# Kernel tuning notes

Hardware: AMD Instinct MI355X
Metric: run time of the kernel (lower is better)

The kernel has to match this reference:

```python
import jax, jax.numpy as jnp
import numpy as np

B, S, H, E, K = 2, 2048, 1024, 8, 2
CAP_FACTOR = 1.5

def setup_inputs() -> dict:
    key = jax.random.key(0)
    ks = jax.random.split(key, 8)
    sd1 = 1.0 / np.sqrt(H)
    sd2 = 1.0 / np.sqrt(H + E)
    return {
        'hidden_states': jax.random.normal(ks[0], (B, S, H), dtype=jnp.float32),
        'w1': jax.random.normal(ks[1], (H, H), dtype=jnp.float32) * sd1,
        'b1': jnp.zeros((H,), jnp.float32),
        'w2': jax.random.normal(ks[2], (H, E), dtype=jnp.float32) * sd1,
        'b2': jnp.zeros((E,), jnp.float32),
        'wc1': jax.random.normal(ks[3], (H + E, H), dtype=jnp.float32) * sd2,
        'bc1': jnp.zeros((H,), jnp.float32),
        'wc2': jax.random.normal(ks[4], (H, E), dtype=jnp.float32) * sd1,
        'bc2': jnp.zeros((E,), jnp.float32),
        'cache_hit_rates': jax.random.uniform(ks[5], (E,), dtype=jnp.float32),
    }

def reference(hidden_states, w1, b1, w2, b2, wc1, bc1, wc2, bc2, cache_hit_rates):
    b, s, h = hidden_states.shape
    # router MLP: Linear -> ReLU -> Linear
    router_logits = jax.nn.relu(hidden_states @ w1 + b1) @ w2 + b2  # [B,S,E]
    # cache-aware adjustment
    avg_features = hidden_states.mean(axis=1)  # [B,H]
    combined = jnp.concatenate(
        [avg_features, jnp.broadcast_to(cache_hit_rates[None, :], (b, E))], axis=-1)
    adj = jnp.tanh(jax.nn.relu(combined @ wc1 + bc1) @ wc2 + bc2)  # [B,E]
    router_logits = router_logits + adj[:, None, :]
    router_probs = jax.nn.softmax(router_logits, axis=-1)  # [B,S,E]
    top_k_probs, top_k_indices = jax.lax.top_k(router_probs, K)  # [B,S,K]
    top_k_probs = top_k_probs / (top_k_probs.sum(axis=-1, keepdims=True) + 1e-8)
    capacity = int(b * s * CAP_FACTOR * K / E)
    # flatten in (b, s, k) order to replicate serial capacity counters
    N = b * s * K
    e_flat = top_k_indices.reshape(N)
    p_flat = top_k_probs.reshape(N)
    tok = jnp.arange(N) // K  # token index b*S+s
    onehot = jax.nn.one_hot(e_flat, E, dtype=jnp.int32)  # [N,E] small
    prior = jnp.cumsum(onehot, axis=0) - onehot  # exclusive count per expert
    pos = prior[jnp.arange(N), e_flat]  # slot within expert
    keep = pos < capacity
    posc = jnp.minimum(pos, capacity - 1)
    val = keep.astype(router_probs.dtype)
    dispatch = jnp.zeros((b * s, E, capacity), router_probs.dtype)
    dispatch = dispatch.at[tok, e_flat, posc].add(val).reshape(b, s, E, capacity)
    combine = jnp.zeros((b * s, E, capacity), router_probs.dtype)
    combine = combine.at[tok, e_flat, posc].add(val * p_flat).reshape(b, s, E, capacity)
    # load balancing aux loss
    router_prob_per_expert = router_probs.mean(axis=(0, 1))  # [E]
    expert_usage_rate = onehot.astype(router_probs.dtype).mean(axis=0)  # [E]
    aux_loss = jnp.sum(router_prob_per_expert * expert_usage_rate) * E
    return dispatch, combine, router_probs, aux_loss
```

## Files before the change

### kernel.cpp

```cpp
#include <hip/hip_runtime.h>
#include <hip/hip_bf16.h>

#define BB 2
#define SS 2048
#define HH 1024
#define EE 8
#define KK 2
#define CAP 1536
#define NTOK (BB * SS)
#define NASSIGN (NTOK * KK)

#define WS_PSUM   0
#define WS_AVG    8
#define WS_HC     2056
#define WS_ADJ    4104
#define WS_P1     4120
#define WS_P2     8216
#define WS_IDX    12312
#define WS_LOGITS 16408
#define WS_ZERO_BYTES 16448
#define WS_BF16_BYTE 196704
#define WS_H_BYTE (WS_BF16_BYTE + 31457280)
#define WS_NEED (WS_H_BYTE + 16777216ull)

using short8 = __attribute__((ext_vector_type(8))) short;
using u16x8  = __attribute__((ext_vector_type(8))) unsigned short;
using f32x4  = __attribute__((ext_vector_type(4))) float;

__device__ __forceinline__ unsigned short f2bf(float f) {
  unsigned u = __float_as_uint(f);
  unsigned r = (u + 0x7fffu + ((u >> 16) & 1u)) >> 16;
  return (unsigned short)r;
}
__device__ __forceinline__ float bf2f(unsigned short h) {
  return __uint_as_float((unsigned)h << 16);
}
__device__ __forceinline__ void split3(float x, unsigned short& h,
                                       unsigned short& m, unsigned short& l) {
  h = f2bf(x);
  float r = x - bf2f(h);
  m = f2bf(r);
  l = f2bf(r - bf2f(m));
}

__device__ __forceinline__ void gload_lds16(const void* g, void* l) {
  __builtin_amdgcn_global_load_lds(
      (const __attribute__((address_space(1))) void*)g,
      (__attribute__((address_space(3))) void*)l, 16, 0, 0);
}

__global__ void k_prep_x(const float* __restrict__ x, unsigned short* __restrict__ Xh,
                         unsigned short* __restrict__ Xm, unsigned short* __restrict__ Xl) {
  int i = (blockIdx.x * 256 + threadIdx.x) * 4;
  float4 v = *(const float4*)&x[i];
  unsigned short h[4], m[4], l[4];
  split3(v.x, h[0], m[0], l[0]);
  split3(v.y, h[1], m[1], l[1]);
  split3(v.z, h[2], m[2], l[2]);
  split3(v.w, h[3], m[3], l[3]);
  *(ushort4*)&Xh[i] = make_ushort4(h[0], h[1], h[2], h[3]);
  *(ushort4*)&Xm[i] = make_ushort4(m[0], m[1], m[2], m[3]);
  *(ushort4*)&Xl[i] = make_ushort4(l[0], l[1], l[2], l[3]);
}

__global__ __launch_bounds__(256) void k_prep_w(const float* __restrict__ w1,
    unsigned short* __restrict__ Wh, unsigned short* __restrict__ Wm,
    unsigned short* __restrict__ Wl) {
  __shared__ unsigned short Th[64 * 65], Tm[64 * 65], Tl[64 * 65];
  int tid = threadIdx.x;
  int k0 = blockIdx.x * 64, n0 = blockIdx.y * 64;
  for (int i = 0; i < 16; ++i) {
    int e = i * 256 + tid;
    int k = e >> 6, n = e & 63;
    float v = w1[(size_t)(k0 + k) * HH + n0 + n];
    unsigned short h, m, l;
    split3(v, h, m, l);
    Th[n * 65 + k] = h; Tm[n * 65 + k] = m; Tl[n * 65 + k] = l;
  }
  __syncthreads();
  for (int i = 0; i < 16; ++i) {
    int e = i * 256 + tid;
    int n = e >> 6, k = e & 63;
    size_t o = (size_t)(n0 + n) * HH + k0 + k;
    Wh[o] = Th[n * 65 + k]; Wm[o] = Tm[n * 65 + k]; Wl[o] = Tl[n * 65 + k];
  }
}

__global__ void k_avg(const float* __restrict__ x, float* __restrict__ avg) {
  int h = blockIdx.x * 256 + threadIdx.x;
  int s0 = blockIdx.y * 128;
  int b = blockIdx.z;
  const float* p = x + (size_t)b * SS * HH + (size_t)s0 * HH + h;
  float s = 0.f;
  for (int i = 0; i < 128; ++i) s += p[(size_t)i * HH];
  atomicAdd(&avg[b * HH + h], s);
}

__global__ void k_hc(const float* __restrict__ avg, const float* __restrict__ chr,
                     const float* __restrict__ wc1, float* __restrict__ hc_raw) {
  int j = blockIdx.x * 256 + threadIdx.x;
  int c = blockIdx.y;
  int b = blockIdx.z;
  const float invS = 1.0f / SS;
  float acc = 0.f;
  const float* a = avg + b * HH;
  for (int i = c * 128; i < c * 128 + 128; ++i)
    acc += (a[i] * invS) * wc1[(size_t)i * HH + j];
  if (c == 7)
    for (int i = 0; i < EE; ++i)
      acc += chr[i] * wc1[(size_t)(HH + i) * HH + j];
  atomicAdd(&hc_raw[b * HH + j], acc);
}

__global__ void k_adj(const float* __restrict__ hc_raw, const float* __restrict__ bc1,
                      const float* __restrict__ wc2, const float* __restrict__ bc2,
                      float* __restrict__ adj) {
  int b = blockIdx.x;
  int tid = threadIdx.x;
  float part[EE] = {};
  for (int j = tid; j < HH; j += 256) {
    float v = fmaxf(hc_raw[b * HH + j] + bc1[j], 0.f);
    for (int e = 0; e < EE; ++e) part[e] += v * wc2[j * EE + e];
  }
  for (int m = 1; m < 64; m <<= 1)
    for (int e = 0; e < EE; ++e) part[e] += __shfl_xor(part[e], m);
  __shared__ float red[4][EE];
  int wave = tid >> 6, lane = tid & 63;
  if (lane == 0)
    for (int e = 0; e < EE; ++e) red[wave][e] = part[e];
  __syncthreads();
  if (tid < EE) {
    float s = bc2[tid];
    for (int w = 0; w < 4; ++w) s += red[w][tid];
    adj[b * EE + tid] = tanhf(s);
  }
}

#define BM 128
#define BN 64
#define BK 32
#define ZF4_PER_BLOCK 49152
__global__ __launch_bounds__(256) void k_gemm_mfma(
    const unsigned short* __restrict__ Xh, const unsigned short* __restrict__ Xm,
    const unsigned short* __restrict__ Xl,
    const unsigned short* __restrict__ Wh, const unsigned short* __restrict__ Wm,
    const unsigned short* __restrict__ Wl,
    const float* __restrict__ b1, float* __restrict__ hbuf,
    f32x4* __restrict__ zout) {
  __shared__ unsigned short As[3][BM * BK];
  __shared__ unsigned short Bs[3][BN * BK];
  __shared__ float b1s[BN];
  int tid = threadIdx.x;
  int m0 = blockIdx.x * BM, n0 = blockIdx.y * BN;
  if (tid < BN) b1s[tid] = b1[n0 + tid];

  int bid = blockIdx.y * gridDim.x + blockIdx.x;
  f32x4* zp = zout + (size_t)bid * ZF4_PER_BLOCK;
  const f32x4 z4 = {0.f, 0.f, 0.f, 0.f};

  int lane = tid & 63, wave = tid >> 6;
  int wm = wave & 1, wn = wave >> 1;
  int q = lane >> 4, mr = lane & 15;
  int lr = lane >> 2, lq = lane & 3;

  f32x4 acc[4][2] = {};

  const unsigned short* Ag[3] = {Xh, Xm, Xl};
  const unsigned short* Bg[3] = {Wh, Wm, Wl};

  for (int k0 = 0; k0 < HH; k0 += BK) {
    __syncthreads();
#pragma unroll
    for (int j = 0; j < 6; ++j) {
      int i = wave + 4 * j;
      int s = i >> 3, g = i & 7;
      const unsigned short* gp =
          Ag[s] + (size_t)(m0 + g * 16 + lr) * HH + k0 + lq * 8;
      gload_lds16(gp, &As[s][g * 512]);
    }
#pragma unroll
    for (int j = 0; j < 3; ++j) {
      int i = wave + 4 * j;
      int s = i >> 2, g = i & 3;
      const unsigned short* gp =
          Bg[s] + (size_t)(n0 + g * 16 + lr) * HH + k0 + lq * 8;
      gload_lds16(gp, &Bs[s][g * 512]);
    }
    __syncthreads();

    {
      int ki = k0 >> 5;
      f32x4* zb = zp + ki * (256 * 6) + tid;
#pragma unroll
      for (int j = 0; j < 6; ++j) __builtin_nontemporal_store(z4, &zb[j * 256]);
    }

    short8 af[3][4], bf[3][2];
#pragma unroll
    for (int s = 0; s < 3; ++s) {
#pragma unroll
      for (int mi = 0; mi < 4; ++mi)
        af[s][mi] = *(const short8*)&As[s][(wm * 64 + mi * 16 + mr) * BK + q * 8];
#pragma unroll
      for (int ni = 0; ni < 2; ++ni)
        bf[s][ni] = *(const short8*)&Bs[s][(wn * 32 + ni * 16 + mr) * BK + q * 8];
    }
#pragma unroll
    for (int mi = 0; mi < 4; ++mi)
#pragma unroll
      for (int ni = 0; ni < 2; ++ni) {
        f32x4 c = acc[mi][ni];
        c = __builtin_amdgcn_mfma_f32_16x16x32_bf16(af[0][mi], bf[0][ni], c, 0, 0, 0);
        c = __builtin_amdgcn_mfma_f32_16x16x32_bf16(af[0][mi], bf[1][ni], c, 0, 0, 0);
        c = __builtin_amdgcn_mfma_f32_16x16x32_bf16(af[1][mi], bf[0][ni], c, 0, 0, 0);
        c = __builtin_amdgcn_mfma_f32_16x16x32_bf16(af[0][mi], bf[2][ni], c, 0, 0, 0);
        c = __builtin_amdgcn_mfma_f32_16x16x32_bf16(af[2][mi], bf[0][ni], c, 0, 0, 0);
        c = __builtin_amdgcn_mfma_f32_16x16x32_bf16(af[1][mi], bf[1][ni], c, 0, 0, 0);
        acc[mi][ni] = c;
      }
  }

#pragma unroll
  for (int ni = 0; ni < 2; ++ni) {
    int cloc = wn * 32 + ni * 16 + mr;
    int col = n0 + cloc;
    float bv = b1s[cloc];
#pragma unroll
    for (int mi = 0; mi < 4; ++mi)
#pragma unroll
      for (int r = 0; r < 4; ++r) {
        int row = m0 + wm * 64 + mi * 16 + q * 4 + r;
        hbuf[(size_t)row * HH + col] = fmaxf(acc[mi][ni][r] + bv, 0.f);
      }
  }
}

__global__ __launch_bounds__(256) void k_logits(
    const float* __restrict__ h, const float* __restrict__ w2,
    const float* __restrict__ b2, const float* __restrict__ adj,
    float* __restrict__ probs_out, int* __restrict__ idx_pack,
    float* __restrict__ p1o, float* __restrict__ p2o, float* __restrict__ psum) {
  __shared__ float w2s[HH * EE];
  __shared__ float ps[EE];
  int tid = threadIdx.x;
#pragma unroll
  for (int j = 0; j < 8; ++j)
    ((float4*)w2s)[tid + 256 * j] = ((const float4*)w2)[tid + 256 * j];
  if (tid < EE) ps[tid] = 0.f;
  __syncthreads();

  int lane = tid & 63, wave = tid >> 6;
  int t = blockIdx.x * 4 + wave;
  float acc[EE] = {};
  const float* hr = h + (size_t)t * HH;
#pragma unroll
  for (int i = 0; i < 16; ++i) {
    int e = lane + 64 * i;
    float hv = hr[e];
    float4 wa = ((const float4*)w2s)[2 * e];
    float4 wb = ((const float4*)w2s)[2 * e + 1];
    acc[0] += hv * wa.x; acc[1] += hv * wa.y; acc[2] += hv * wa.z; acc[3] += hv * wa.w;
    acc[4] += hv * wb.x; acc[5] += hv * wb.y; acc[6] += hv * wb.z; acc[7] += hv * wb.w;
  }
#pragma unroll
  for (int m = 1; m < 64; m <<= 1)
#pragma unroll
    for (int e = 0; e < EE; ++e) acc[e] += __shfl_xor(acc[e], m);

  if (lane == 0) {
    int b = t >> 11;
    float l[EE];
    float mx = -1e30f;
    for (int e = 0; e < EE; ++e) {
      l[e] = acc[e] + b2[e] + adj[b * EE + e];
      mx = fmaxf(mx, l[e]);
    }
    float s = 0.f;
    for (int e = 0; e < EE; ++e) { l[e] = expf(l[e] - mx); s += l[e]; }
    float inv = 1.f / s;
    for (int e = 0; e < EE; ++e) { l[e] *= inv; probs_out[t * EE + e] = l[e]; }
    int e1 = 0; float p1 = l[0];
    for (int e = 1; e < EE; ++e) if (l[e] > p1) { p1 = l[e]; e1 = e; }
    int e2 = -1; float p2 = -1.f;
    for (int e = 0; e < EE; ++e) if (e != e1 && l[e] > p2) { p2 = l[e]; e2 = e; }
    float norm = 1.f / (p1 + p2 + 1e-8f);
    idx_pack[t] = e1 | (e2 << 8);
    p1o[t] = p1 * norm;
    p2o[t] = p2 * norm;
    for (int e = 0; e < EE; ++e) atomicAdd(&ps[e], l[e]);
  }
  __syncthreads();
  if (tid < EE) atomicAdd(&psum[tid], ps[tid]);
}

__global__ __launch_bounds__(256) void k_gemm_f32(
    const float* __restrict__ X, const float* __restrict__ w1,
    const float* __restrict__ b1, const float* __restrict__ w2,
    float* __restrict__ logits) {
  __shared__ float Asf[16][65];
  __shared__ float Bsf[16][64];
  __shared__ float w2sf[64][EE];
  int tid = threadIdx.x;
  int m0 = blockIdx.x * 64, n0 = blockIdx.y * 64;
  for (int i = tid; i < 64 * EE; i += 256)
    w2sf[i / EE][i % EE] = w2[(size_t)(n0 + i / EE) * EE + (i % EE)];
  float acc[4][4] = {};
  int tx = tid & 15, ty = tid >> 4;
  for (int k0 = 0; k0 < HH; k0 += 16) {
    for (int idx = tid; idx < 64 * 16; idx += 256) {
      int m = idx >> 4, kk = idx & 15;
      Asf[kk][m] = X[(size_t)(m0 + m) * HH + k0 + kk];
    }
    for (int idx = tid; idx < 16 * 64; idx += 256) {
      int kk = idx >> 6, n = idx & 63;
      Bsf[kk][n] = w1[(size_t)(k0 + kk) * HH + n0 + n];
    }
    __syncthreads();
    for (int kk = 0; kk < 16; ++kk) {
      float a[4], bb[4];
      for (int i = 0; i < 4; ++i) a[i] = Asf[kk][ty * 4 + i];
      for (int j = 0; j < 4; ++j) bb[j] = Bsf[kk][tx * 4 + j];
      for (int i = 0; i < 4; ++i)
        for (int j = 0; j < 4; ++j) acc[i][j] += a[i] * bb[j];
    }
    __syncthreads();
  }
  float p[4][EE] = {};
  for (int i = 0; i < 4; ++i)
    for (int j = 0; j < 4; ++j) {
      int c = tx * 4 + j;
      float v = fmaxf(acc[i][j] + b1[n0 + c], 0.f);
      for (int e = 0; e < EE; ++e) p[i][e] += v * w2sf[c][e];
    }
  for (int m = 1; m < 16; m <<= 1)
    for (int i = 0; i < 4; ++i)
      for (int e = 0; e < EE; ++e) p[i][e] += __shfl_xor(p[i][e], m);
  if (tx == 0)
    for (int i = 0; i < 4; ++i)
      for (int e = 0; e < EE; ++e)
        atomicAdd(&logits[(size_t)(m0 + ty * 4 + i) * EE + e], p[i][e]);
}

__global__ void k_init_logits(const float* __restrict__ adj, const float* __restrict__ b2,
                              float* __restrict__ logits) {
  int i = blockIdx.x * 256 + threadIdx.x;
  int e = i & 7;
  int t = i >> 3;
  int b = t >> 11;
  logits[i] = b2[e] + adj[b * EE + e];
}

__global__ void k_softmax(const float* __restrict__ logits, float* __restrict__ probs_out,
                          int* __restrict__ idx_pack, float* __restrict__ p1o,
                          float* __restrict__ p2o, float* __restrict__ psum) {
  int t = blockIdx.x * 256 + threadIdx.x;
  float l[EE];
  float mx = -1e30f;
  for (int e = 0; e < EE; ++e) { l[e] = logits[t * EE + e]; mx = fmaxf(mx, l[e]); }
  float s = 0.f;
  for (int e = 0; e < EE; ++e) { l[e] = expf(l[e] - mx); s += l[e]; }
  float inv = 1.f / s;
  for (int e = 0; e < EE; ++e) { l[e] *= inv; probs_out[t * EE + e] = l[e]; }
  int e1 = 0; float p1 = l[0];
  for (int e = 1; e < EE; ++e) if (l[e] > p1) { p1 = l[e]; e1 = e; }
  int e2 = -1; float p2 = -1.f;
  for (int e = 0; e < EE; ++e) if (e != e1 && l[e] > p2) { p2 = l[e]; e2 = e; }
  float norm = 1.f / (p1 + p2 + 1e-8f);
  idx_pack[t] = e1 | (e2 << 8);
  p1o[t] = p1 * norm;
  p2o[t] = p2 * norm;
  for (int m = 1; m < 64; m <<= 1)
    for (int e = 0; e < EE; ++e) l[e] += __shfl_xor(l[e], m);
  if ((threadIdx.x & 63) == 0)
    for (int e = 0; e < EE; ++e) atomicAdd(&psum[e], l[e]);
}

__global__ __launch_bounds__(256) void k_route(
    const int* __restrict__ idx_pack, const float* __restrict__ p1,
    const float* __restrict__ p2, const float* __restrict__ psum,
    float* __restrict__ disp, float* __restrict__ comb, float* __restrict__ aux_out) {
  __shared__ int cnt[256][EE];
  __shared__ int tot[EE];
  int tid = threadIdx.x;
  const int CH = NASSIGN / 256;
  int n0 = tid * CH;
  int local[EE] = {};
  for (int n = n0; n < n0 + CH; ++n) {
    int t = n >> 1;
    int pk = idx_pack[t];
    int e = (n & 1) ? (pk >> 8) : (pk & 0xff);
    local[e]++;
  }
  for (int e = 0; e < EE; ++e) cnt[tid][e] = local[e];
  __syncthreads();
  if (tid < EE) {
    int run = 0;
    for (int t = 0; t < 256; ++t) { int v = cnt[t][tid]; cnt[t][tid] = run; run += v; }
    tot[tid] = run;
  }
  __syncthreads();
  int off[EE];
  for (int e = 0; e < EE; ++e) off[e] = cnt[tid][e];
  for (int n = n0; n < n0 + CH; ++n) {
    int t = n >> 1;
    int pk = idx_pack[t];
    int e; float p;
    if (n & 1) { e = pk >> 8; p = p2[t]; } else { e = pk & 0xff; p = p1[t]; }
    int pos = off[e]++;
    if (pos < CAP) {
      size_t o = (size_t)t * EE * CAP + (size_t)e * CAP + pos;
      disp[o] = 1.0f;
      comb[o] = p;
    }
  }
  if (tid == 0) {
    float aux = 0.f;
    for (int e = 0; e < EE; ++e)
      aux += (psum[e] / (float)NTOK) * ((float)tot[e] / (float)NASSIGN);
    aux_out[0] = aux * (float)EE;
  }
}

extern "C" void kernel_launch(void* const* d_in, const int* in_sizes, int n_in,
                              void* d_out, int out_size, void* d_ws, size_t ws_size,
                              hipStream_t stream) {
  const float* x   = (const float*)d_in[0];
  const float* w1  = (const float*)d_in[1];
  const float* b1  = (const float*)d_in[2];
  const float* w2  = (const float*)d_in[3];
  const float* b2  = (const float*)d_in[4];
  const float* wc1 = (const float*)d_in[5];
  const float* bc1 = (const float*)d_in[6];
  const float* wc2 = (const float*)d_in[7];
  const float* bc2 = (const float*)d_in[8];
  const float* chr = (const float*)d_in[9];

  float* out = (float*)d_out;
  float* disp  = out;
  float* comb  = disp + (size_t)NTOK * EE * CAP;
  float* probs = comb + (size_t)NTOK * EE * CAP;
  float* aux   = probs + (size_t)NTOK * EE;

  float* ws = (float*)d_ws;
  float* psum   = ws + WS_PSUM;
  float* avg    = ws + WS_AVG;
  float* hcr    = ws + WS_HC;
  float* adj    = ws + WS_ADJ;
  float* p1     = ws + WS_P1;
  float* p2     = ws + WS_P2;
  int*   idxp   = (int*)(ws + WS_IDX);
  float* logits = ws + WS_LOGITS;

  char* wsb = (char*)d_ws;
  unsigned short* Xh = (unsigned short*)(wsb + WS_BF16_BYTE);
  unsigned short* Xm = Xh + (size_t)NTOK * HH;
  unsigned short* Xl = Xm + (size_t)NTOK * HH;
  unsigned short* Wh = Xl + (size_t)NTOK * HH;
  unsigned short* Wm = Wh + (size_t)HH * HH;
  unsigned short* Wl = Wm + (size_t)HH * HH;
  float* hbuf = (float*)(wsb + WS_H_BYTE);

  hipMemsetAsync(d_ws, 0, WS_ZERO_BYTES, stream);

  bool use_mfma = ws_size >= WS_NEED;

  if (use_mfma) {
    k_prep_x<<<(NTOK * HH) / (4 * 256), 256, 0, stream>>>(x, Xh, Xm, Xl);
    k_prep_w<<<dim3(HH / 64, HH / 64), 256, 0, stream>>>(w1, Wh, Wm, Wl);
  }
  k_avg<<<dim3(HH / 256, SS / 128, BB), 256, 0, stream>>>(x, avg);
  k_hc<<<dim3(HH / 256, 8, BB), 256, 0, stream>>>(avg, chr, wc1, hcr);
  k_adj<<<BB, 256, 0, stream>>>(hcr, bc1, wc2, bc2, adj);
  if (use_mfma) {
    k_gemm_mfma<<<dim3(NTOK / BM, HH / BN), 256, 0, stream>>>(
        Xh, Xm, Xl, Wh, Wm, Wl, b1, hbuf, (f32x4*)d_out);
    k_logits<<<NTOK / 4, 256, 0, stream>>>(hbuf, w2, b2, adj, probs, idxp, p1, p2, psum);
  } else {
    hipMemsetAsync(d_out, 0, (size_t)out_size * sizeof(float), stream);
    k_init_logits<<<(NTOK * EE) / 256, 256, 0, stream>>>(adj, b2, logits);
    k_gemm_f32<<<dim3(NTOK / 64, HH / 64), 256, 0, stream>>>(x, w1, b1, w2, logits);
    k_softmax<<<NTOK / 256, 256, 0, stream>>>(logits, probs, idxp, p1, p2, psum);
  }
  k_route<<<1, 256, 0, stream>>>(idxp, p1, p2, psum, disp, comb, aux);
}
```

Measured before the change: 524.1 us.

## Move output zeroing into dedicated GEMM blocks and batch logits per wave

The big nontemporal zero-fill of the dispatch/combine outputs no longer runs inside the GEMM k-loop. It now runs in 8 extra grid rows of zero-only blocks that execute alongside the MFMA blocks. The workspace-header memset is folded into block 0 of k_prep_x, and k_logits now handles 4 tokens per wave so fewer blocks each reload w2 into LDS. A 3-blocks-per-SM launch bound is added to the GEMM, which may raise register pressure or cause spills.

```diff
diff --git a/kernel.cpp b/kernel.cpp
--- a/kernel.cpp
+++ b/kernel.cpp
@@ -18,6 +18,7 @@
 #define WS_P2     8216
 #define WS_IDX    12312
 #define WS_LOGITS 16408
+#define WS_ZERO_FLOATS 4112
 #define WS_ZERO_BYTES 16448
 #define WS_BF16_BYTE 196704
 #define WS_H_BYTE (WS_BF16_BYTE + 31457280)
@@ -50,8 +51,12 @@
 }
 
 __global__ void k_prep_x(const float* __restrict__ x, unsigned short* __restrict__ Xh,
-                         unsigned short* __restrict__ Xm, unsigned short* __restrict__ Xl) {
-  int i = (blockIdx.x * 256 + threadIdx.x) * 4;
+                         unsigned short* __restrict__ Xm, unsigned short* __restrict__ Xl,
+                         float* __restrict__ wshead) {
+  int tid = threadIdx.x;
+  if (blockIdx.x == 0)
+    for (int j = tid; j < WS_ZERO_FLOATS; j += 256) wshead[j] = 0.f;
+  int i = (blockIdx.x * 256 + tid) * 4;
   float4 v = *(const float4*)&x[i];
   unsigned short h[4], m[4], l[4];
   split3(v.x, h[0], m[0], l[0]);
@@ -139,8 +144,8 @@
 #define BM 128
 #define BN 64
 #define BK 32
-#define ZF4_PER_BLOCK 49152
-__global__ __launch_bounds__(256) void k_gemm_mfma(
+#define ZF4_PER_ZBLOCK 98304
+__global__ __launch_bounds__(256, 3) void k_gemm_mfma(
     const unsigned short* __restrict__ Xh, const unsigned short* __restrict__ Xm,
     const unsigned short* __restrict__ Xl,
     const unsigned short* __restrict__ Wh, const unsigned short* __restrict__ Wm,
@@ -151,12 +156,19 @@
   __shared__ unsigned short Bs[3][BN * BK];
   __shared__ float b1s[BN];
   int tid = threadIdx.x;
+
+  if (blockIdx.y >= HH / BN) {
+    int zb = (blockIdx.y - HH / BN) * gridDim.x + blockIdx.x;
+    f32x4* zp = zout + (size_t)zb * ZF4_PER_ZBLOCK + tid;
+    const f32x4 z4 = {0.f, 0.f, 0.f, 0.f};
+#pragma unroll 8
+    for (int j = 0; j < ZF4_PER_ZBLOCK / 256; ++j)
+      __builtin_nontemporal_store(z4, &zp[j * 256]);
+    return;
+  }
+
   int m0 = blockIdx.x * BM, n0 = blockIdx.y * BN;
   if (tid < BN) b1s[tid] = b1[n0 + tid];
-
-  int bid = blockIdx.y * gridDim.x + blockIdx.x;
-  f32x4* zp = zout + (size_t)bid * ZF4_PER_BLOCK;
-  const f32x4 z4 = {0.f, 0.f, 0.f, 0.f};
 
   int lane = tid & 63, wave = tid >> 6;
   int wm = wave & 1, wn = wave >> 1;
@@ -187,13 +199,6 @@
       gload_lds16(gp, &Bs[s][g * 512]);
     }
     __syncthreads();
-
-    {
-      int ki = k0 >> 5;
-      f32x4* zb = zp + ki * (256 * 6) + tid;
-#pragma unroll
-      for (int j = 0; j < 6; ++j) __builtin_nontemporal_store(z4, &zb[j * 256]);
-    }
 
     short8 af[3][4], bf[3][2];
 #pragma unroll
@@ -250,44 +255,47 @@
   __syncthreads();
 
   int lane = tid & 63, wave = tid >> 6;
-  int t = blockIdx.x * 4 + wave;
-  float acc[EE] = {};
-  const float* hr = h + (size_t)t * HH;
-#pragma unroll
-  for (int i = 0; i < 16; ++i) {
-    int e = lane + 64 * i;
-    float hv = hr[e];
-    float4 wa = ((const float4*)w2s)[2 * e];
-    float4 wb = ((const float4*)w2s)[2 * e + 1];
-    acc[0] += hv * wa.x; acc[1] += hv * wa.y; acc[2] += hv * wa.z; acc[3] += hv * wa.w;
-    acc[4] += hv * wb.x; acc[5] += hv * wb.y; acc[6] += hv * wb.z; acc[7] += hv * wb.w;
-  }
-#pragma unroll
-  for (int m = 1; m < 64; m <<= 1)
-#pragma unroll
-    for (int e = 0; e < EE; ++e) acc[e] += __shfl_xor(acc[e], m);
-
-  if (lane == 0) {
-    int b = t >> 11;
-    float l[EE];
-    float mx = -1e30f;
-    for (int e = 0; e < EE; ++e) {
-      l[e] = acc[e] + b2[e] + adj[b * EE + e];
-      mx = fmaxf(mx, l[e]);
-    }
-    float s = 0.f;
-    for (int e = 0; e < EE; ++e) { l[e] = expf(l[e] - mx); s += l[e]; }
-    float inv = 1.f / s;
-    for (int e = 0; e < EE; ++e) { l[e] *= inv; probs_out[t * EE + e] = l[e]; }
-    int e1 = 0; float p1 = l[0];
-    for (int e = 1; e < EE; ++e) if (l[e] > p1) { p1 = l[e]; e1 = e; }
-    int e2 = -1; float p2 = -1.f;
-    for (int e = 0; e < EE; ++e) if (e != e1 && l[e] > p2) { p2 = l[e]; e2 = e; }
-    float norm = 1.f / (p1 + p2 + 1e-8f);
-    idx_pack[t] = e1 | (e2 << 8);
-    p1o[t] = p1 * norm;
-    p2o[t] = p2 * norm;
-    for (int e = 0; e < EE; ++e) atomicAdd(&ps[e], l[e]);
+#pragma unroll
+  for (int ti = 0; ti < 4; ++ti) {
+    int t = blockIdx.x * 16 + wave * 4 + ti;
+    float acc[EE] = {};
+    const float* hr = h + (size_t)t * HH;
+#pragma unroll
+    for (int i = 0; i < 16; ++i) {
+      int e = lane + 64 * i;
+      float hv = hr[e];
+      float4 wa = ((const float4*)w2s)[2 * e];
+      float4 wb = ((const float4*)w2s)[2 * e + 1];
+      acc[0] += hv * wa.x; acc[1] += hv * wa.y; acc[2] += hv * wa.z; acc[3] += hv * wa.w;
+      acc[4] += hv * wb.x; acc[5] += hv * wb.y; acc[6] += hv * wb.z; acc[7] += hv * wb.w;
+    }
+#pragma unroll
+    for (int m = 1; m < 64; m <<= 1)
+#pragma unroll
+      for (int e = 0; e < EE; ++e) acc[e] += __shfl_xor(acc[e], m);
+
+    if (lane == 0) {
+      int b = t >> 11;
+      float l[EE];
+      float mx = -1e30f;
+      for (int e = 0; e < EE; ++e) {
+        l[e] = acc[e] + b2[e] + adj[b * EE + e];
+        mx = fmaxf(mx, l[e]);
+      }
+      float s = 0.f;
+      for (int e = 0; e < EE; ++e) { l[e] = expf(l[e] - mx); s += l[e]; }
+      float inv = 1.f / s;
+      for (int e = 0; e < EE; ++e) { l[e] *= inv; probs_out[t * EE + e] = l[e]; }
+      int e1 = 0; float p1 = l[0];
+      for (int e = 1; e < EE; ++e) if (l[e] > p1) { p1 = l[e]; e1 = e; }
+      int e2 = -1; float p2 = -1.f;
+      for (int e = 0; e < EE; ++e) if (e != e1 && l[e] > p2) { p2 = l[e]; e2 = e; }
+      float norm = 1.f / (p1 + p2 + 1e-8f);
+      idx_pack[t] = e1 | (e2 << 8);
+      p1o[t] = p1 * norm;
+      p2o[t] = p2 * norm;
+      for (int e = 0; e < EE; ++e) atomicAdd(&ps[e], l[e]);
+    }
   }
   __syncthreads();
   if (tid < EE) atomicAdd(&psum[tid], ps[tid]);
@@ -460,21 +468,21 @@
   unsigned short* Wl = Wm + (size_t)HH * HH;
   float* hbuf = (float*)(wsb + WS_H_BYTE);
 
-  hipMemsetAsync(d_ws, 0, WS_ZERO_BYTES, stream);
-
   bool use_mfma = ws_size >= WS_NEED;
 
   if (use_mfma) {
-    k_prep_x<<<(NTOK * HH) / (4 * 256), 256, 0, stream>>>(x, Xh, Xm, Xl);
+    k_prep_x<<<(NTOK * HH) / (4 * 256), 256, 0, stream>>>(x, Xh, Xm, Xl, ws);
     k_prep_w<<<dim3(HH / 64, HH / 64), 256, 0, stream>>>(w1, Wh, Wm, Wl);
+  } else {
+    hipMemsetAsync(d_ws, 0, WS_ZERO_BYTES, stream);
   }
   k_avg<<<dim3(HH / 256, SS / 128, BB), 256, 0, stream>>>(x, avg);
   k_hc<<<dim3(HH / 256, 8, BB), 256, 0, stream>>>(avg, chr, wc1, hcr);
   k_adj<<<BB, 256, 0, stream>>>(hcr, bc1, wc2, bc2, adj);
   if (use_mfma) {
-    k_gemm_mfma<<<dim3(NTOK / BM, HH / BN), 256, 0, stream>>>(
+    k_gemm_mfma<<<dim3(NTOK / BM, HH / BN + 8), 256, 0, stream>>>(
         Xh, Xm, Xl, Wh, Wm, Wl, b1, hbuf, (f32x4*)d_out);
-    k_logits<<<NTOK / 4, 256, 0, stream>>>(hbuf, w2, b2, adj, probs, idxp, p1, p2, psum);
+    k_logits<<<NTOK / 16, 256, 0, stream>>>(hbuf, w2, b2, adj, probs, idxp, p1, p2, psum);
   } else {
     hipMemsetAsync(d_out, 0, (size_t)out_size * sizeof(float), stream);
     k_init_logits<<<(NTOK * EE) / 256, 256, 0, stream>>>(adj, b2, logits);
```

After: 530.4 us. No clear change (+1.2%).

## Fuse prep, averaging and memset launches; fold adj into GEMM grid

Applied to the files above, without the earlier changes.

Merges the X split, W split-and-transpose and sequence-mean kernels into one launch, partitioned by block index. Block 0 of that launch zeroes the workspace head, which removes the separate memset. The mean now writes per-chunk partials, which k_hc reduces in shared memory, instead of using atomics. The small tanh-adjust computation runs as an extra grid row of the MFMA GEMM kernel rather than its own launch. Together this cuts kernel launches and serialization gaps, at the cost of a heterogeneous fused kernel and some idle early-exit blocks.

```diff
diff --git a/kernel.cpp b/kernel.cpp
--- a/kernel.cpp
+++ b/kernel.cpp
@@ -18,6 +18,7 @@
 #define WS_P2     8216
 #define WS_IDX    12312
 #define WS_LOGITS 16408
+#define WS_ZERO_FLOATS 4112
 #define WS_ZERO_BYTES 16448
 #define WS_BF16_BYTE 196704
 #define WS_H_BYTE (WS_BF16_BYTE + 31457280)
@@ -49,63 +50,89 @@
       (__attribute__((address_space(3))) void*)l, 16, 0, 0);
 }
 
-__global__ void k_prep_x(const float* __restrict__ x, unsigned short* __restrict__ Xh,
-                         unsigned short* __restrict__ Xm, unsigned short* __restrict__ Xl) {
-  int i = (blockIdx.x * 256 + threadIdx.x) * 4;
-  float4 v = *(const float4*)&x[i];
-  unsigned short h[4], m[4], l[4];
-  split3(v.x, h[0], m[0], l[0]);
-  split3(v.y, h[1], m[1], l[1]);
-  split3(v.z, h[2], m[2], l[2]);
-  split3(v.w, h[3], m[3], l[3]);
-  *(ushort4*)&Xh[i] = make_ushort4(h[0], h[1], h[2], h[3]);
-  *(ushort4*)&Xm[i] = make_ushort4(m[0], m[1], m[2], m[3]);
-  *(ushort4*)&Xl[i] = make_ushort4(l[0], l[1], l[2], l[3]);
-}
-
-__global__ __launch_bounds__(256) void k_prep_w(const float* __restrict__ w1,
+#define PREPX_BLKS 4096
+#define PREPW_BLKS 256
+#define AVG_BLKS   128
+__global__ __launch_bounds__(256) void k_prep(
+    const float* __restrict__ x, const float* __restrict__ w1,
+    unsigned short* __restrict__ Xh, unsigned short* __restrict__ Xm,
+    unsigned short* __restrict__ Xl,
     unsigned short* __restrict__ Wh, unsigned short* __restrict__ Wm,
-    unsigned short* __restrict__ Wl) {
+    unsigned short* __restrict__ Wl,
+    float* __restrict__ wshead, float* __restrict__ avg_part) {
   __shared__ unsigned short Th[64 * 65], Tm[64 * 65], Tl[64 * 65];
   int tid = threadIdx.x;
-  int k0 = blockIdx.x * 64, n0 = blockIdx.y * 64;
-  for (int i = 0; i < 16; ++i) {
-    int e = i * 256 + tid;
-    int k = e >> 6, n = e & 63;
-    float v = w1[(size_t)(k0 + k) * HH + n0 + n];
-    unsigned short h, m, l;
-    split3(v, h, m, l);
-    Th[n * 65 + k] = h; Tm[n * 65 + k] = m; Tl[n * 65 + k] = l;
-  }
-  __syncthreads();
-  for (int i = 0; i < 16; ++i) {
-    int e = i * 256 + tid;
-    int n = e >> 6, k = e & 63;
-    size_t o = (size_t)(n0 + n) * HH + k0 + k;
-    Wh[o] = Th[n * 65 + k]; Wm[o] = Tm[n * 65 + k]; Wl[o] = Tl[n * 65 + k];
-  }
-}
-
-__global__ void k_avg(const float* __restrict__ x, float* __restrict__ avg) {
+  int bid = blockIdx.x;
+  if (bid < PREPX_BLKS) {
+    if (bid == 0)
+      for (int j = tid; j < WS_ZERO_FLOATS; j += 256) wshead[j] = 0.f;
+    int i = (bid * 256 + tid) * 4;
+    float4 v = *(const float4*)&x[i];
+    unsigned short h[4], m[4], l[4];
+    split3(v.x, h[0], m[0], l[0]);
+    split3(v.y, h[1], m[1], l[1]);
+    split3(v.z, h[2], m[2], l[2]);
+    split3(v.w, h[3], m[3], l[3]);
+    *(ushort4*)&Xh[i] = make_ushort4(h[0], h[1], h[2], h[3]);
+    *(ushort4*)&Xm[i] = make_ushort4(m[0], m[1], m[2], m[3]);
+    *(ushort4*)&Xl[i] = make_ushort4(l[0], l[1], l[2], l[3]);
+  } else if (bid < PREPX_BLKS + PREPW_BLKS) {
+    int pid = bid - PREPX_BLKS;
+    int k0 = (pid & 15) * 64, n0 = (pid >> 4) * 64;
+    for (int i = 0; i < 16; ++i) {
+      int e = i * 256 + tid;
+      int k = e >> 6, n = e & 63;
+      float v = w1[(size_t)(k0 + k) * HH + n0 + n];
+      unsigned short h, m, l;
+      split3(v, h, m, l);
+      Th[n * 65 + k] = h; Tm[n * 65 + k] = m; Tl[n * 65 + k] = l;
+    }
+    __syncthreads();
+    for (int i = 0; i < 16; ++i) {
+      int e = i * 256 + tid;
+      int n = e >> 6, k = e & 63;
+      size_t o = (size_t)(n0 + n) * HH + k0 + k;
+      Wh[o] = Th[n * 65 + k]; Wm[o] = Tm[n * 65 + k]; Wl[o] = Tl[n * 65 + k];
+    }
+  } else {
+    int pid = bid - PREPX_BLKS - PREPW_BLKS;
+    int h = (pid & 3) * 256 + tid;
+    int c = (pid >> 2) & 15;
+    int b = pid >> 6;
+    const float* p = x + (size_t)b * SS * HH + (size_t)(c * 128) * HH + h;
+    float s = 0.f;
+    for (int i = 0; i < 128; ++i) s += p[(size_t)i * HH];
+    avg_part[(c * BB + b) * HH + h] = s;
+  }
+}
+
+__global__ void k_avgp(const float* __restrict__ x, float* __restrict__ avg_part) {
   int h = blockIdx.x * 256 + threadIdx.x;
-  int s0 = blockIdx.y * 128;
+  int c = blockIdx.y;
   int b = blockIdx.z;
-  const float* p = x + (size_t)b * SS * HH + (size_t)s0 * HH + h;
+  const float* p = x + (size_t)b * SS * HH + (size_t)(c * 128) * HH + h;
   float s = 0.f;
   for (int i = 0; i < 128; ++i) s += p[(size_t)i * HH];
-  atomicAdd(&avg[b * HH + h], s);
-}
-
-__global__ void k_hc(const float* __restrict__ avg, const float* __restrict__ chr,
+  avg_part[(c * BB + b) * HH + h] = s;
+}
+
+__global__ void k_hc(const float* __restrict__ avg_part, const float* __restrict__ chr,
                      const float* __restrict__ wc1, float* __restrict__ hc_raw) {
-  int j = blockIdx.x * 256 + threadIdx.x;
+  __shared__ float avg_s[128];
+  int tid = threadIdx.x;
+  int j = blockIdx.x * 256 + tid;
   int c = blockIdx.y;
   int b = blockIdx.z;
-  const float invS = 1.0f / SS;
+  if (tid < 128) {
+    float s = 0.f;
+    for (int cc = 0; cc < 16; ++cc)
+      s += avg_part[(cc * BB + b) * HH + c * 128 + tid];
+    avg_s[tid] = s * (1.0f / SS);
+  }
+  __syncthreads();
   float acc = 0.f;
-  const float* a = avg + b * HH;
-  for (int i = c * 128; i < c * 128 + 128; ++i)
-    acc += (a[i] * invS) * wc1[(size_t)i * HH + j];
+  for (int il = 0; il < 128; ++il)
+    acc += avg_s[il] * wc1[(size_t)(c * 128 + il) * HH + j];
   if (c == 7)
     for (int i = 0; i < EE; ++i)
       acc += chr[i] * wc1[(size_t)(HH + i) * HH + j];
@@ -146,11 +173,38 @@
     const unsigned short* __restrict__ Wh, const unsigned short* __restrict__ Wm,
     const unsigned short* __restrict__ Wl,
     const float* __restrict__ b1, float* __restrict__ hbuf,
-    f32x4* __restrict__ zout) {
+    f32x4* __restrict__ zout,
+    const float* __restrict__ hc_raw, const float* __restrict__ bc1,
+    const float* __restrict__ wc2, const float* __restrict__ bc2,
+    float* __restrict__ adj) {
   __shared__ unsigned short As[3][BM * BK];
   __shared__ unsigned short Bs[3][BN * BK];
   __shared__ float b1s[BN];
-  int tid = threadIdx.x;
+  __shared__ float red[4][EE];
+  int tid = threadIdx.x;
+
+  if (blockIdx.y == HH / BN) {
+    if (blockIdx.x >= BB) return;
+    int b = blockIdx.x;
+    float part[EE] = {};
+    for (int j = tid; j < HH; j += 256) {
+      float v = fmaxf(hc_raw[b * HH + j] + bc1[j], 0.f);
+      for (int e = 0; e < EE; ++e) part[e] += v * wc2[j * EE + e];
+    }
+    for (int m = 1; m < 64; m <<= 1)
+      for (int e = 0; e < EE; ++e) part[e] += __shfl_xor(part[e], m);
+    int wave = tid >> 6, lane = tid & 63;
+    if (lane == 0)
+      for (int e = 0; e < EE; ++e) red[wave][e] = part[e];
+    __syncthreads();
+    if (tid < EE) {
+      float s = bc2[tid];
+      for (int w = 0; w < 4; ++w) s += red[w][tid];
+      adj[b * EE + tid] = tanhf(s);
+    }
+    return;
+  }
+
   int m0 = blockIdx.x * BM, n0 = blockIdx.y * BN;
   if (tid < BN) b1s[tid] = b1[n0 + tid];
 
@@ -443,13 +497,13 @@
 
   float* ws = (float*)d_ws;
   float* psum   = ws + WS_PSUM;
-  float* avg    = ws + WS_AVG;
   float* hcr    = ws + WS_HC;
   float* adj    = ws + WS_ADJ;
   float* p1     = ws + WS_P1;
   float* p2     = ws + WS_P2;
   int*   idxp   = (int*)(ws + WS_IDX);
   float* logits = ws + WS_LOGITS;
+  float* avgp   = ws + WS_LOGITS;
 
   char* wsb = (char*)d_ws;
   unsigned short* Xh = (unsigned short*)(wsb + WS_BF16_BYTE);
@@ -460,23 +514,22 @@
   unsigned short* Wl = Wm + (size_t)HH * HH;
   float* hbuf = (float*)(wsb + WS_H_BYTE);
 
-  hipMemsetAsync(d_ws, 0, WS_ZERO_BYTES, stream);
-
   bool use_mfma = ws_size >= WS_NEED;
 
   if (use_mfma) {
-    k_prep_x<<<(NTOK * HH) / (4 * 256), 256, 0, stream>>>(x, Xh, Xm, Xl);
-    k_prep_w<<<dim3(HH / 64, HH / 64), 256, 0, stream>>>(w1, Wh, Wm, Wl);
-  }
-  k_avg<<<dim3(HH / 256, SS / 128, BB), 256, 0, stream>>>(x, avg);
-  k_hc<<<dim3(HH / 256, 8, BB), 256, 0, stream>>>(avg, chr, wc1, hcr);
-  k_adj<<<BB, 256, 0, stream>>>(hcr, bc1, wc2, bc2, adj);
-  if (use_mfma) {
-    k_gemm_mfma<<<dim3(NTOK / BM, HH / BN), 256, 0, stream>>>(
-        Xh, Xm, Xl, Wh, Wm, Wl, b1, hbuf, (f32x4*)d_out);
+    k_prep<<<PREPX_BLKS + PREPW_BLKS + AVG_BLKS, 256, 0, stream>>>(
+        x, w1, Xh, Xm, Xl, Wh, Wm, Wl, ws, avgp);
+    k_hc<<<dim3(HH / 256, 8, BB), 256, 0, stream>>>(avgp, chr, wc1, hcr);
+    k_gemm_mfma<<<dim3(NTOK / BM, HH / BN + 1), 256, 0, stream>>>(
+        Xh, Xm, Xl, Wh, Wm, Wl, b1, hbuf, (f32x4*)d_out,
+        hcr, bc1, wc2, bc2, adj);
     k_logits<<<NTOK / 4, 256, 0, stream>>>(hbuf, w2, b2, adj, probs, idxp, p1, p2, psum);
   } else {
+    hipMemsetAsync(d_ws, 0, WS_ZERO_BYTES, stream);
     hipMemsetAsync(d_out, 0, (size_t)out_size * sizeof(float), stream);
+    k_avgp<<<dim3(HH / 256, 16, BB), 256, 0, stream>>>(x, avgp);
+    k_hc<<<dim3(HH / 256, 8, BB), 256, 0, stream>>>(avgp, chr, wc1, hcr);
+    k_adj<<<BB, 256, 0, stream>>>(hcr, bc1, wc2, bc2, adj);
     k_init_logits<<<(NTOK * EE) / 256, 256, 0, stream>>>(adj, b2, logits);
     k_gemm_f32<<<dim3(NTOK / 64, HH / 64), 256, 0, stream>>>(x, w1, b1, w2, logits);
     k_softmax<<<NTOK / 256, 256, 0, stream>>>(logits, probs, idxp, p1, p2, psum);
```

Result: faster. 509.3 us (-2.8%).
